# Performance work log

Hardware: AMD Instinct MI355X
Metric: run time of the kernel (lower is better)

Reference implementation:

```python
import jax, jax.numpy as jnp
import numpy as np
import math

B, N, E, H = 16, 1024, 512, 8
DH = E // H

def setup_inputs() -> dict:
    key = jax.random.key(0)
    ks = jax.random.split(key, 12)
    inp = {
        "q": jax.random.normal(ks[0], (B, N, E), dtype=jnp.float32),
        "k": jax.random.normal(ks[1], (B, N, E), dtype=jnp.float32),
        "v": jax.random.normal(ks[2], (B, N, E), dtype=jnp.float32),
        "d": jax.random.uniform(ks[3], (B, N, N), dtype=jnp.float32),
        # nn.Linear weights (out, in) with orthogonal-ish init scaled small, zero bias
        "Wq": jax.random.normal(ks[4], (E, E), dtype=jnp.float32) * 0.01,
        "bq": jnp.zeros((E,), dtype=jnp.float32),
        "Wk": jax.random.normal(ks[5], (E, E), dtype=jnp.float32) * 0.01,
        "bk": jnp.zeros((E,), dtype=jnp.float32),
        "Wv": jax.random.normal(ks[6], (E, E), dtype=jnp.float32) * 0.01,
        "bv": jnp.zeros((E,), dtype=jnp.float32),
        "Wp": jax.random.normal(ks[7], (E, E), dtype=jnp.float32) * 0.01,
        "bp": jnp.zeros((E,), dtype=jnp.float32),
    }
    return inp

def _heads(x, W, b):
    # torch Linear: x @ W.T + b, then split heads -> [B, H, N, DH]
    y = jnp.einsum('bne,fe->bnf', x, W) + b
    return y.reshape(x.shape[0], x.shape[1], H, DH).transpose(0, 2, 1, 3)

def reference(q, k, v, d, Wq, bq, Wk, bk, Wv, bv, Wp, bp):
    qh = _heads(q, Wq, bq)                                  # [B,H,N,DH]
    kh = _heads(k, Wk, bk)
    vh = _heads(v, Wv, bv)
    scale = 1.0 / math.sqrt(DH)
    att = jnp.einsum('bhnd,bhmd->bhnm', qh, kh) * scale     # [B,H,N,N]
    db = d[:, None, :, :]                                   # broadcast over heads
    att = jax.nn.softmax(att + db, axis=-1)
    att = att * db                                          # multiplicative distance bias post-softmax
    x = jnp.einsum('bhnm,bhmd->bhnd', att, vh)              # [B,H,N,DH]
    x = x.transpose(0, 2, 1, 3).reshape(q.shape[0], q.shape[1], E)
    return jnp.einsum('bne,fe->bnf', x, Wp) + bp
```

## Files before the change

### kernel.cpp

```cpp
#include <hip/hip_runtime.h>
#include <hip/hip_bf16.h>


#define Bc  16
#define Nc  1024
#define Ec  512
#define Hc  8
#define DHc 64

typedef float  f32x4  __attribute__((ext_vector_type(4)));
typedef short  s16x4  __attribute__((ext_vector_type(4)));
typedef short  s16x8  __attribute__((ext_vector_type(8)));
typedef __bf16 bf16x8 __attribute__((ext_vector_type(8)));

static __device__ __forceinline__ f32x4 mfma16(s16x8 a, s16x8 b, f32x4 c) {
    return __builtin_amdgcn_mfma_f32_16x16x32_bf16(
        __builtin_bit_cast(bf16x8, a), __builtin_bit_cast(bf16x8, b), c, 0, 0, 0);
}

static __device__ __forceinline__ unsigned short f2bf(float f) {
    return __builtin_bit_cast(unsigned short, __float2bfloat16(f));
}

static __device__ __forceinline__ s16x8 pack_bf16(f32x4 a, f32x4 b) {
    s16x8 r;
    r[0] = (short)f2bf(a[0]); r[1] = (short)f2bf(a[1]);
    r[2] = (short)f2bf(a[2]); r[3] = (short)f2bf(a[3]);
    r[4] = (short)f2bf(b[0]); r[5] = (short)f2bf(b[1]);
    r[6] = (short)f2bf(b[2]); r[7] = (short)f2bf(b[3]);
    return r;
}

static __device__ __forceinline__ void gld16(const void* g, void* l) {
    __builtin_amdgcn_global_load_lds(
        (const __attribute__((address_space(1))) void*)g,
        (__attribute__((address_space(3))) void*)l, 16, 0, 0);
}

__global__ __launch_bounds__(256) void proj3_kernel(
    const float* __restrict__ qi, const float* __restrict__ ki,
    const float* __restrict__ vi,
    const float* __restrict__ Wq, const float* __restrict__ Wk,
    const float* __restrict__ Wv,
    const float* __restrict__ bq, const float* __restrict__ bk,
    const float* __restrict__ bv,
    unsigned short* __restrict__ qo, unsigned short* __restrict__ ko,
    unsigned short* __restrict__ vo)
{
    const int z = blockIdx.z;
    const float* Af   = z == 0 ? qi : (z == 1 ? ki : vi);
    const float* Wm   = z == 0 ? Wq : (z == 1 ? Wk : Wv);
    const float* bias = z == 0 ? bq : (z == 1 ? bk : bv);
    unsigned short* out = z == 0 ? qo : (z == 1 ? ko : vo);
    const int mode = (z == 2) ? 1 : 0;

    __shared__ float Bs[128 * 32];
    __shared__ float As_raw[128 * 32];

    const int tid = threadIdx.x;
    const int w = tid >> 6, lane = tid & 63;
    const int lr = lane & 15, grp = lane >> 4;
    const int wr = w >> 1, wc = w & 1;
    const int m0 = blockIdx.x * 128, n0 = blockIdx.y * 128;

    f32x4 acc[4][4];
#pragma unroll
    for (int i = 0; i < 4; ++i)
#pragma unroll
        for (int j = 0; j < 4; ++j) acc[i][j] = (f32x4)(0.0f);

    const int h8 = lane >> 3, l8 = lane & 7;
    const int fcol = ((l8 ^ h8) << 2);
    const int o0 = (((grp << 1) ^ (lr & 7)) << 2);

    for (int k0 = 0; k0 < Ec; k0 += 32) {
        __syncthreads();
#pragma unroll
        for (int i = 0; i < 4; ++i) {
            const int chunk = i * 4 + w;
            const int row = chunk * 8 + h8;
            gld16(Wm + (size_t)(n0 + row) * Ec + k0 + fcol,
                  (char*)Bs + chunk * 1024 + lane * 16);
            gld16(Af + (size_t)(m0 + row) * Ec + k0 + fcol,
                  (char*)As_raw + chunk * 1024 + lane * 16);
        }
        __syncthreads();

        s16x8 afr[4], bfr[4];
#pragma unroll
        for (int mi = 0; mi < 4; ++mi) {
            const float* p = As_raw + (wr * 64 + mi * 16 + lr) * 32;
            afr[mi] = pack_bf16(*(const f32x4*)(p + o0), *(const f32x4*)(p + (o0 ^ 4)));
        }
#pragma unroll
        for (int ni = 0; ni < 4; ++ni) {
            const float* p = Bs + (wc * 64 + ni * 16 + lr) * 32;
            bfr[ni] = pack_bf16(*(const f32x4*)(p + o0), *(const f32x4*)(p + (o0 ^ 4)));
        }
#pragma unroll
        for (int mi = 0; mi < 4; ++mi)
#pragma unroll
            for (int ni = 0; ni < 4; ++ni)
                acc[mi][ni] = mfma16(afr[mi], bfr[ni], acc[mi][ni]);
    }

#pragma unroll
    for (int mi = 0; mi < 4; ++mi) {
        const int mbase = m0 + wr * 64 + mi * 16 + grp * 4;
#pragma unroll
        for (int ni = 0; ni < 4; ++ni) {
            const int f = n0 + wc * 64 + ni * 16 + lr;
            const float bi = bias[f];
            f32x4 vv = acc[mi][ni];
            const int hh = f >> 6, dh = f & 63;
            if (mode == 0) {
#pragma unroll
                for (int r = 0; r < 4; ++r) {
                    const int m = mbase + r;
                    out[(((size_t)(m >> 10) * Hc + hh) * Nc + (m & (Nc - 1))) * DHc + dh] =
                        f2bf(vv[r] + bi);
                }
            } else {
                const int bb = mbase >> 10, n = mbase & (Nc - 1);
                s16x4 pk;
#pragma unroll
                for (int r = 0; r < 4; ++r) pk[r] = (short)f2bf(vv[r] + bi);
                *(s16x4*)&out[(((size_t)bb * Hc + hh) * DHc + dh) * Nc + n] = pk;
            }
        }
    }
}

__global__ __launch_bounds__(256) void outproj_kernel(
    const unsigned short* __restrict__ Ab, const float* __restrict__ Wm,
    const float* __restrict__ bias, float* __restrict__ out)
{
    __shared__ float Bs[128 * 32];
    __shared__ unsigned short Asb[128 * 32];

    const int tid = threadIdx.x;
    const int w = tid >> 6, lane = tid & 63;
    const int lr = lane & 15, grp = lane >> 4;
    const int wr = w >> 1, wc = w & 1;
    const int m0 = blockIdx.x * 128, n0 = blockIdx.y * 128;

    f32x4 acc[4][4];
#pragma unroll
    for (int i = 0; i < 4; ++i)
#pragma unroll
        for (int j = 0; j < 4; ++j) acc[i][j] = (f32x4)(0.0f);

    const int h8 = lane >> 3, l8 = lane & 7;
    const int fcol = ((l8 ^ h8) << 2);
    const int h4 = lane >> 2, l4 = lane & 3;
    const int bcol = ((l4 ^ (h4 & 3)) << 3);
    const int o0 = (((grp << 1) ^ (lr & 7)) << 2);
    const int ob = ((grp ^ (lr & 3)) << 3);

    for (int k0 = 0; k0 < Ec; k0 += 32) {
        __syncthreads();
#pragma unroll
        for (int i = 0; i < 4; ++i) {
            const int chunk = i * 4 + w;
            const int row = chunk * 8 + h8;
            gld16(Wm + (size_t)(n0 + row) * Ec + k0 + fcol,
                  (char*)Bs + chunk * 1024 + lane * 16);
        }
#pragma unroll
        for (int i = 0; i < 2; ++i) {
            const int chunk = i * 4 + w;
            const int row = chunk * 16 + h4;
            gld16(Ab + (size_t)(m0 + row) * Ec + k0 + bcol,
                  (char*)Asb + chunk * 1024 + lane * 16);
        }
        __syncthreads();

        s16x8 afr[4], bfr[4];
#pragma unroll
        for (int mi = 0; mi < 4; ++mi)
            afr[mi] = *(const s16x8*)(Asb + (wr * 64 + mi * 16 + lr) * 32 + ob);
#pragma unroll
        for (int ni = 0; ni < 4; ++ni) {
            const float* p = Bs + (wc * 64 + ni * 16 + lr) * 32;
            bfr[ni] = pack_bf16(*(const f32x4*)(p + o0), *(const f32x4*)(p + (o0 ^ 4)));
        }
#pragma unroll
        for (int mi = 0; mi < 4; ++mi)
#pragma unroll
            for (int ni = 0; ni < 4; ++ni)
                acc[mi][ni] = mfma16(afr[mi], bfr[ni], acc[mi][ni]);
    }

#pragma unroll
    for (int mi = 0; mi < 4; ++mi) {
        const int mbase = m0 + wr * 64 + mi * 16 + grp * 4;
#pragma unroll
        for (int ni = 0; ni < 4; ++ni) {
            const int f = n0 + wc * 64 + ni * 16 + lr;
            const float bi = bias[f];
            f32x4 vv = acc[mi][ni];
#pragma unroll
            for (int r = 0; r < 4; ++r)
                out[(size_t)(mbase + r) * Ec + f] = vv[r] + bi;
        }
    }
}

__global__ __launch_bounds__(512) void attn_kernel(
    const unsigned short* __restrict__ qh, const unsigned short* __restrict__ kh,
    const unsigned short* __restrict__ vt, const float* __restrict__ dmat,
    unsigned short* __restrict__ xh)
{
    __shared__ unsigned short K_lds[64 * 64];
    __shared__ unsigned short V_lds[64 * 64];
    __shared__ unsigned short P_lds[8][16][72];

    const int lin = blockIdx.x;
    const int swz = ((lin & 7) << 7) | (lin >> 3);
    const int qt = swz & 7, h = (swz >> 3) & 7, b = swz >> 6;

    const int tid = threadIdx.x;
    const int w = tid >> 6, lane = tid & 63;
    const int lr = lane & 15, grp = lane >> 4;
    const int h8 = lane >> 3, l8 = lane & 7;
    const int q0 = qt * 128;
    const int bh = b * Hc + h;
    const int qw = q0 + w * 16;
    const int kofs = grp * 4;
    const int scol = (l8 ^ h8) * 8;
    const float* dbase = dmat + ((size_t)b * Nc + qw + lr) * Nc;

    const float LOG2E = 1.4426950408889634f;
    const float SC    = 0.125f * LOG2E;
    const float MC    = -4.0f * LOG2E;

    s16x8 bq[2];
#pragma unroll
    for (int ks = 0; ks < 2; ++ks)
        bq[ks] = *reinterpret_cast<const s16x8*>(
            qh + ((size_t)bh * Nc + qw + lr) * DHc + ks * 32 + grp * 8);

    f32x4 acc[4];
#pragma unroll
    for (int c = 0; c < 4; ++c) acc[c] = (f32x4)(0.0f);
    float lsum = 0.f;

    for (int kt = 0; kt < Nc / 64; ++kt) {
        const int k0 = kt * 64;
        __syncthreads();
        gld16(kh + ((size_t)bh * Nc + k0 + w * 8 + h8) * DHc + scol,
              (char*)K_lds + w * 1024 + lane * 16);
        gld16(vt + ((size_t)bh * DHc + w * 8 + h8) * Nc + k0 + scol,
              (char*)V_lds + w * 1024 + lane * 16);
        f32x4 dv[4];
#pragma unroll
        for (int c = 0; c < 4; ++c)
            dv[c] = *reinterpret_cast<const f32x4*>(dbase + k0 + c * 16 + kofs);
        __syncthreads();

        f32x4 lgt[4];
#pragma unroll
        for (int c = 0; c < 4; ++c) lgt[c] = (f32x4)(0.0f);
#pragma unroll
        for (int ks = 0; ks < 2; ++ks) {
#pragma unroll
            for (int c = 0; c < 4; ++c) {
                const int row = c * 16 + lr;
                const int slot = (4 * ks + grp) ^ (lr & 7);
                s16x8 ak = *reinterpret_cast<const s16x8*>(
                    (const char*)K_lds + row * 128 + slot * 16);
                lgt[c] = mfma16(ak, bq[ks], lgt[c]);
            }
        }
#pragma unroll
        for (int c = 0; c < 4; ++c) {
            s16x4 pk;
#pragma unroll
            for (int r = 0; r < 4; ++r) {
                const float dl = fmaf(dv[c][r], LOG2E, MC);
                const float p = __builtin_amdgcn_exp2f(fmaf(lgt[c][r], SC, dl));
                lsum += p;
                pk[r] = (short)f2bf(p * dv[c][r]);
            }
            *reinterpret_cast<s16x4*>(&P_lds[w][lr][c * 16 + kofs]) = pk;
        }
#pragma unroll
        for (int ks = 0; ks < 2; ++ks) {
            s16x8 pa = *reinterpret_cast<const s16x8*>(&P_lds[w][lr][ks * 32 + grp * 8]);
#pragma unroll
            for (int c = 0; c < 4; ++c) {
                const int row = c * 16 + lr;
                const int slot = (4 * ks + grp) ^ (lr & 7);
                s16x8 bv = *reinterpret_cast<const s16x8*>(
                    (const char*)V_lds + row * 128 + slot * 16);
                acc[c] = mfma16(pa, bv, acc[c]);
            }
        }
    }
    lsum += __shfl_xor(lsum, 16, 64);
    lsum += __shfl_xor(lsum, 32, 64);
    const float invd = 1.0f / lsum;
    float inv[4];
#pragma unroll
    for (int r = 0; r < 4; ++r) inv[r] = __shfl(invd, grp * 4 + r, 64);
#pragma unroll
    for (int c = 0; c < 4; ++c)
#pragma unroll
        for (int r = 0; r < 4; ++r)
            xh[((size_t)b * Nc + qw + grp * 4 + r) * Ec + h * DHc + c * 16 + lr] =
                f2bf(acc[c][r] * inv[r]);
}

extern "C" void kernel_launch(void* const* d_in, const int* in_sizes, int n_in,
                              void* d_out, int out_size, void* d_ws, size_t ws_size,
                              hipStream_t stream)
{
    (void)in_sizes; (void)n_in; (void)out_size; (void)ws_size;
    const float* q  = (const float*)d_in[0];
    const float* k  = (const float*)d_in[1];
    const float* v  = (const float*)d_in[2];
    const float* dm = (const float*)d_in[3];
    const float* Wq = (const float*)d_in[4];
    const float* bq = (const float*)d_in[5];
    const float* Wk = (const float*)d_in[6];
    const float* bk = (const float*)d_in[7];
    const float* Wv = (const float*)d_in[8];
    const float* bv = (const float*)d_in[9];
    const float* Wp = (const float*)d_in[10];
    const float* bp = (const float*)d_in[11];
    float* out = (float*)d_out;

    const size_t sz = (size_t)Bc * Hc * Nc * DHc;
    unsigned short* qhb = (unsigned short*)d_ws;
    unsigned short* khb = qhb + sz;
    unsigned short* vtb = khb + sz;
    unsigned short* xhb = vtb + sz;

    proj3_kernel<<<dim3(Bc * Nc / 128, Ec / 128, 3), dim3(256), 0, stream>>>(
        q, k, v, Wq, Wk, Wv, bq, bk, bv, qhb, khb, vtb);
    attn_kernel<<<dim3(Bc * Hc * Nc / 128), dim3(512), 0, stream>>>(
        qhb, khb, vtb, dm, xhb);
    outproj_kernel<<<dim3(Bc * Nc / 128, Ec / 128), dim3(256), 0, stream>>>(
        xhb, Wp, bp, out);
}
```

Measured before the change: 180.8 us.

## Pre-convert weights to bf16 and load V fragments directly from global

Adds a small kernel that converts all four weight matrices to bf16 once per call, so the projection GEMMs load half the bytes for B tiles and skip per-tile fp32-to-bf16 packing. In the attention kernel, V is no longer staged through LDS; each lane reads its V fragments straight from global memory, removing one async LDS copy and the LDS reads. This costs an extra kernel launch and workspace, and the direct V loads may be less coalesced or add latency to the inner loop.

```diff
diff --git a/kernel.cpp b/kernel.cpp
--- a/kernel.cpp
+++ b/kernel.cpp
@@ -37,25 +37,36 @@
         (__attribute__((address_space(3))) void*)l, 16, 0, 0);
 }
 
+__global__ __launch_bounds__(256) void wcvt_kernel(
+    const float* __restrict__ Wq, const float* __restrict__ Wk,
+    const float* __restrict__ Wv, const float* __restrict__ Wp,
+    unsigned short* __restrict__ wbf)
+{
+    const int seg = blockIdx.x >> 7;
+    const float* src = seg == 0 ? Wq : (seg == 1 ? Wk : (seg == 2 ? Wv : Wp));
+    const int g = (blockIdx.x & 127) * 256 + threadIdx.x;
+    const float* p = src + (size_t)g * 8;
+    f32x4 a = *(const f32x4*)p, b = *(const f32x4*)(p + 4);
+    *(s16x8*)(wbf + (size_t)seg * 262144 + (size_t)g * 8) = pack_bf16(a, b);
+}
+
 __global__ __launch_bounds__(256) void proj3_kernel(
     const float* __restrict__ qi, const float* __restrict__ ki,
-    const float* __restrict__ vi,
-    const float* __restrict__ Wq, const float* __restrict__ Wk,
-    const float* __restrict__ Wv,
+    const float* __restrict__ vi, const unsigned short* __restrict__ wbf,
     const float* __restrict__ bq, const float* __restrict__ bk,
     const float* __restrict__ bv,
     unsigned short* __restrict__ qo, unsigned short* __restrict__ ko,
     unsigned short* __restrict__ vo)
 {
     const int z = blockIdx.z;
-    const float* Af   = z == 0 ? qi : (z == 1 ? ki : vi);
-    const float* Wm   = z == 0 ? Wq : (z == 1 ? Wk : Wv);
+    const float* Af = z == 0 ? qi : (z == 1 ? ki : vi);
+    const unsigned short* Wb = wbf + (size_t)z * 262144;
     const float* bias = z == 0 ? bq : (z == 1 ? bk : bv);
     unsigned short* out = z == 0 ? qo : (z == 1 ? ko : vo);
     const int mode = (z == 2) ? 1 : 0;
 
-    __shared__ float Bs[128 * 32];
     __shared__ float As_raw[128 * 32];
+    __shared__ unsigned short Bsb[128 * 32];
 
     const int tid = threadIdx.x;
     const int w = tid >> 6, lane = tid & 63;
@@ -71,7 +82,10 @@
 
     const int h8 = lane >> 3, l8 = lane & 7;
     const int fcol = ((l8 ^ h8) << 2);
+    const int h4 = lane >> 2, l4 = lane & 3;
+    const int bcol = ((l4 ^ (h4 & 3)) << 3);
     const int o0 = (((grp << 1) ^ (lr & 7)) << 2);
+    const int ob = ((grp ^ (lr & 3)) << 3);
 
     for (int k0 = 0; k0 < Ec; k0 += 32) {
         __syncthreads();
@@ -79,10 +93,15 @@
         for (int i = 0; i < 4; ++i) {
             const int chunk = i * 4 + w;
             const int row = chunk * 8 + h8;
-            gld16(Wm + (size_t)(n0 + row) * Ec + k0 + fcol,
-                  (char*)Bs + chunk * 1024 + lane * 16);
             gld16(Af + (size_t)(m0 + row) * Ec + k0 + fcol,
                   (char*)As_raw + chunk * 1024 + lane * 16);
+        }
+#pragma unroll
+        for (int i = 0; i < 2; ++i) {
+            const int chunk = i * 4 + w;
+            const int row = chunk * 16 + h4;
+            gld16(Wb + (size_t)(n0 + row) * Ec + k0 + bcol,
+                  (char*)Bsb + chunk * 1024 + lane * 16);
         }
         __syncthreads();
 
@@ -93,10 +112,8 @@
             afr[mi] = pack_bf16(*(const f32x4*)(p + o0), *(const f32x4*)(p + (o0 ^ 4)));
         }
 #pragma unroll
-        for (int ni = 0; ni < 4; ++ni) {
-            const float* p = Bs + (wc * 64 + ni * 16 + lr) * 32;
-            bfr[ni] = pack_bf16(*(const f32x4*)(p + o0), *(const f32x4*)(p + (o0 ^ 4)));
-        }
+        for (int ni = 0; ni < 4; ++ni)
+            bfr[ni] = *(const s16x8*)(Bsb + (wc * 64 + ni * 16 + lr) * 32 + ob);
 #pragma unroll
         for (int mi = 0; mi < 4; ++mi)
 #pragma unroll
@@ -132,11 +149,11 @@
 }
 
 __global__ __launch_bounds__(256) void outproj_kernel(
-    const unsigned short* __restrict__ Ab, const float* __restrict__ Wm,
+    const unsigned short* __restrict__ Ab, const unsigned short* __restrict__ Wb,
     const float* __restrict__ bias, float* __restrict__ out)
 {
-    __shared__ float Bs[128 * 32];
     __shared__ unsigned short Asb[128 * 32];
+    __shared__ unsigned short Bsb[128 * 32];
 
     const int tid = threadIdx.x;
     const int w = tid >> 6, lane = tid & 63;
@@ -150,28 +167,20 @@
 #pragma unroll
         for (int j = 0; j < 4; ++j) acc[i][j] = (f32x4)(0.0f);
 
-    const int h8 = lane >> 3, l8 = lane & 7;
-    const int fcol = ((l8 ^ h8) << 2);
     const int h4 = lane >> 2, l4 = lane & 3;
     const int bcol = ((l4 ^ (h4 & 3)) << 3);
-    const int o0 = (((grp << 1) ^ (lr & 7)) << 2);
     const int ob = ((grp ^ (lr & 3)) << 3);
 
     for (int k0 = 0; k0 < Ec; k0 += 32) {
         __syncthreads();
-#pragma unroll
-        for (int i = 0; i < 4; ++i) {
-            const int chunk = i * 4 + w;
-            const int row = chunk * 8 + h8;
-            gld16(Wm + (size_t)(n0 + row) * Ec + k0 + fcol,
-                  (char*)Bs + chunk * 1024 + lane * 16);
-        }
 #pragma unroll
         for (int i = 0; i < 2; ++i) {
             const int chunk = i * 4 + w;
             const int row = chunk * 16 + h4;
             gld16(Ab + (size_t)(m0 + row) * Ec + k0 + bcol,
                   (char*)Asb + chunk * 1024 + lane * 16);
+            gld16(Wb + (size_t)(n0 + row) * Ec + k0 + bcol,
+                  (char*)Bsb + chunk * 1024 + lane * 16);
         }
         __syncthreads();
 
@@ -180,10 +189,8 @@
         for (int mi = 0; mi < 4; ++mi)
             afr[mi] = *(const s16x8*)(Asb + (wr * 64 + mi * 16 + lr) * 32 + ob);
 #pragma unroll
-        for (int ni = 0; ni < 4; ++ni) {
-            const float* p = Bs + (wc * 64 + ni * 16 + lr) * 32;
-            bfr[ni] = pack_bf16(*(const f32x4*)(p + o0), *(const f32x4*)(p + (o0 ^ 4)));
-        }
+        for (int ni = 0; ni < 4; ++ni)
+            bfr[ni] = *(const s16x8*)(Bsb + (wc * 64 + ni * 16 + lr) * 32 + ob);
 #pragma unroll
         for (int mi = 0; mi < 4; ++mi)
 #pragma unroll
@@ -212,7 +219,6 @@
     unsigned short* __restrict__ xh)
 {
     __shared__ unsigned short K_lds[64 * 64];
-    __shared__ unsigned short V_lds[64 * 64];
     __shared__ unsigned short P_lds[8][16][72];
 
     const int lin = blockIdx.x;
@@ -250,13 +256,19 @@
         __syncthreads();
         gld16(kh + ((size_t)bh * Nc + k0 + w * 8 + h8) * DHc + scol,
               (char*)K_lds + w * 1024 + lane * 16);
-        gld16(vt + ((size_t)bh * DHc + w * 8 + h8) * Nc + k0 + scol,
-              (char*)V_lds + w * 1024 + lane * 16);
         f32x4 dv[4];
 #pragma unroll
         for (int c = 0; c < 4; ++c)
             dv[c] = *reinterpret_cast<const f32x4*>(dbase + k0 + c * 16 + kofs);
         __syncthreads();
+
+        s16x8 vf[2][4];
+#pragma unroll
+        for (int ks = 0; ks < 2; ++ks)
+#pragma unroll
+            for (int c = 0; c < 4; ++c)
+                vf[ks][c] = *reinterpret_cast<const s16x8*>(
+                    vt + ((size_t)bh * DHc + c * 16 + lr) * Nc + k0 + ks * 32 + grp * 8);
 
         f32x4 lgt[4];
 #pragma unroll
@@ -288,13 +300,8 @@
         for (int ks = 0; ks < 2; ++ks) {
             s16x8 pa = *reinterpret_cast<const s16x8*>(&P_lds[w][lr][ks * 32 + grp * 8]);
 #pragma unroll
-            for (int c = 0; c < 4; ++c) {
-                const int row = c * 16 + lr;
-                const int slot = (4 * ks + grp) ^ (lr & 7);
-                s16x8 bv = *reinterpret_cast<const s16x8*>(
-                    (const char*)V_lds + row * 128 + slot * 16);
-                acc[c] = mfma16(pa, bv, acc[c]);
-            }
+            for (int c = 0; c < 4; ++c)
+                acc[c] = mfma16(pa, vf[ks][c], acc[c]);
         }
     }
     lsum += __shfl_xor(lsum, 16, 64);
@@ -335,11 +342,13 @@
     unsigned short* khb = qhb + sz;
     unsigned short* vtb = khb + sz;
     unsigned short* xhb = vtb + sz;
-
+    unsigned short* wbf = xhb + sz;
+
+    wcvt_kernel<<<dim3(512), dim3(256), 0, stream>>>(Wq, Wk, Wv, Wp, wbf);
     proj3_kernel<<<dim3(Bc * Nc / 128, Ec / 128, 3), dim3(256), 0, stream>>>(
-        q, k, v, Wq, Wk, Wv, bq, bk, bv, qhb, khb, vtb);
+        q, k, v, wbf, bq, bk, bv, qhb, khb, vtb);
     attn_kernel<<<dim3(Bc * Hc * Nc / 128), dim3(512), 0, stream>>>(
         qhb, khb, vtb, dm, xhb);
     outproj_kernel<<<dim3(Bc * Nc / 128, Ec / 128), dim3(256), 0, stream>>>(
-        xhb, Wp, bp, out);
-}
+        xhb, wbf + (size_t)3 * 262144, bp, out);
+}
```

Measured after the change: 255.8 us. +41.5%, slower.
